# Optimization experiments

Measured on AMD Instinct MI355X. Metric: run time of the kernel, lower is better.

Reference implementation:

```python
import jax, jax.numpy as jnp
import numpy as np

N_NODES = 100_000
N_EDGES = 3_200_000
N_FEAT = 128
HIDDEN = 16
OUT = 2
N_GRAPHS = 64


def setup_inputs() -> dict:
    key = jax.random.key(0)
    ks = jax.random.split(key, 12)
    x = jax.random.normal(ks[0], (N_NODES, N_FEAT), dtype=jnp.float32)
    edge_index = jax.random.randint(ks[1], (2, N_EDGES), 0, N_NODES, dtype=jnp.int64)
    batch_idx = jnp.sort(jax.random.randint(ks[2], (N_NODES,), 0, N_GRAPHS, dtype=jnp.int64))

    def glorot(k, shape):
        s = jnp.sqrt(6.0 / (shape[0] + shape[1])).astype(jnp.float32)
        return jax.random.uniform(k, shape, jnp.float32, -1.0, 1.0) * s

    return {
        "x": x, "edge_index": edge_index, "batch_idx": batch_idx,
        "W0": glorot(ks[3], (N_FEAT, HIDDEN)), "b0": jnp.zeros((HIDDEN,), jnp.float32),
        "a0": jnp.full((1,), 0.25, jnp.float32),  # PReLU default weight
        "W1": glorot(ks[4], (HIDDEN, HIDDEN)), "b1": jnp.zeros((HIDDEN,), jnp.float32),
        "a1": jnp.full((1,), 0.25, jnp.float32),
        "W2": glorot(ks[5], (HIDDEN, HIDDEN)), "b2": jnp.zeros((HIDDEN,), jnp.float32),
        "a2": jnp.full((1,), 0.25, jnp.float32),
        "W3": glorot(ks[6], (HIDDEN, OUT)), "b3": jnp.zeros((OUT,), jnp.float32),
    }


def _prelu(x, a):
    return jnp.where(x > 0, x, a * x)


def _gcn_conv(x, W, b, src, dst, norm, n):
    # PyG GCNConv: linear transform, then normalized gather-scatter aggregation, then bias
    h = x @ W                                   # [N, out]
    msg = h[src] * norm[:, None]                # gather + per-edge scale
    out = jax.ops.segment_sum(msg, dst, num_segments=n)  # scatter-add into targets
    return out + b


def reference(x, edge_index, batch_idx, W0, b0, a0, W1, b1, a1, W2, b2, a2, W3, b3):
    n = x.shape[0]
    loop = jnp.arange(n, dtype=edge_index.dtype)
    src = jnp.concatenate([edge_index[0], loop])  # add self loops
    dst = jnp.concatenate([edge_index[1], loop])
    # symmetric degree normalization deg^-1/2 (deg over targets, all edge weights = 1)
    deg = jax.ops.segment_sum(jnp.ones_like(dst, dtype=x.dtype), dst, num_segments=n)
    dinv = jnp.where(deg > 0, jax.lax.rsqrt(deg), 0.0)
    norm = dinv[src] * dinv[dst]

    h = _prelu(_gcn_conv(x, W0, b0, src, dst, norm, n), a0)
    h = _prelu(_gcn_conv(h, W1, b1, src, dst, norm, n), a1)
    h = _prelu(_gcn_conv(h, W2, b2, src, dst, norm, n), a2)
    h = _gcn_conv(h, W3, b3, src, dst, norm, n)

    # global_mean_pool over graph ids
    sums = jax.ops.segment_sum(h, batch_idx, num_segments=N_GRAPHS)
    cnts = jax.ops.segment_sum(jnp.ones((n,), h.dtype), batch_idx, num_segments=N_GRAPHS)
    return sums / jnp.maximum(cnts, 1.0)[:, None]
```

## Files before the change

kernel.cpp:

```cpp
#include <hip/hip_runtime.h>


#define NN 100000
#define NE 3200000
#define NF 128
#define NH 16
#define NO 2
#define NG 64
#define NBLK 391
#define BN 256
#define NBUK 391
#define CHUNK 4096
#define NBLKA 782
#define CAPF 10240
#define NT0 6250

typedef __attribute__((ext_vector_type(8))) short short8;
typedef __attribute__((ext_vector_type(4))) float float4v;


__device__ __forceinline__ float ldf(const void* p, int i, int f32) {
  if (f32) return ((const float*)p)[i];
  unsigned int u = ((const unsigned short*)p)[i];
  return __uint_as_float(u << 16);
}
__device__ __forceinline__ int ldi(const void* p, int i, int i64) {
  if (i64) return (int)((const long long*)p)[i];
  return ((const int*)p)[i];
}
__device__ __forceinline__ void stf(void* p, int i, float v, int f32) {
  if (f32) {
    ((float*)p)[i] = v;
  } else {
    unsigned int w = __float_as_uint(v);
    unsigned int r = (w + 0x7fffu + ((w >> 16) & 1u)) >> 16;
    ((unsigned short*)p)[i] = (unsigned short)r;
  }
}
__device__ __forceinline__ float bf16lo(unsigned int u) { return __uint_as_float(u << 16); }
__device__ __forceinline__ float bf16hi(unsigned int u) { return __uint_as_float(u & 0xffff0000u); }
__device__ __forceinline__ unsigned int packbf(float x, float y) {
  unsigned int a = __float_as_uint(x);
  a = (a + 0x7fffu + ((a >> 16) & 1u)) >> 16;
  unsigned int b = __float_as_uint(y);
  b = (b + 0x7fffu + ((b >> 16) & 1u)) & 0xffff0000u;
  return a | b;
}
__device__ __forceinline__ int okf(float v) { return (v == v) && (fabsf(v) < 1e30f); }
__device__ __forceinline__ void nflag(int* diag, int bad, int bit) {
  if (__any(bad)) {
    if ((threadIdx.x & 63) == 0) atomicOr(diag + 2, 1 << bit);
  }
}
__device__ __forceinline__ int clampi(int v, int hi) {
  return (unsigned)v < (unsigned)hi ? v : 0;
}


__global__ __launch_bounds__(64) void k_sniff(const void* x, const void* ei, int* diag) {
  int lane = threadIdx.x;
  unsigned int xv = ((const unsigned int*)x)[lane];
  unsigned int e = (xv >> 7) & 0xffu;
  int hit = (e >= 116u && e <= 133u);
  int hits = __popcll(__ballot(hit));
  unsigned int ev = ((const unsigned int*)ei)[2 * lane + 1];
  int nzc = __popcll(__ballot(ev != 0u));
  if (lane == 0) {
    diag[0] = (hits < 32) ? 1 : 0;
    diag[1] = (nzc == 0) ? 1 : 0;
  }
}


__global__ __launch_bounds__(256) void k_build(const void* ei, const int* __restrict__ diag,
                                               int* __restrict__ cursor, int* __restrict__ ents) {
  __shared__ int spktA[CHUNK];
  __shared__ unsigned short sbid[CHUNK];
  __shared__ unsigned short srank[CHUNK];
  __shared__ int spktB[CHUNK];
  __shared__ int gpos[CHUNK];
  __shared__ int lscan[512];
  __shared__ int sexcl[NBUK];
  __shared__ int goff[NBUK];
  int tid = threadIdx.x, blk = blockIdx.x;
  lscan[tid] = 0; lscan[tid + 256] = 0;
  __syncthreads();
  int i64 = diag[1];
  int base = blk * CHUNK;
  int n = NE - base; n = n > CHUNK ? CHUNK : n;
  for (int i = tid; i < n; i += 256) {
    int sv = clampi(ldi(ei, base + i, i64), NN);
    int dv = clampi(ldi(ei, NE + base + i, i64), NN);
    int b = dv >> 8;
    spktA[i] = ((dv & 255) << 17) | sv;
    sbid[i] = (unsigned short)b;
    srank[i] = (unsigned short)atomicAdd(&lscan[b], 1);
  }
  __syncthreads();
  for (int off = 1; off < 512; off <<= 1) {
    int v0 = (tid >= off) ? lscan[tid - off] : 0;
    int v1 = lscan[tid + 256 - off];
    __syncthreads();
    lscan[tid] += v0;
    lscan[tid + 256] += v1;
    __syncthreads();
  }
  for (int b = tid; b < NBUK; b += 256) {
    int incl = lscan[b];
    int excl = (b > 0) ? lscan[b - 1] : 0;
    int cnt = incl - excl;
    sexcl[b] = excl;
    int rbase = cnt ? atomicAdd(&cursor[b], cnt) : 0;
    goff[b] = b * CAPF + rbase - excl;
  }
  __syncthreads();
  for (int i = tid; i < n; i += 256) {
    int b = sbid[i];
    int rr = sexcl[b] + srank[i];
    spktB[rr] = spktA[i];
    int gp = goff[b] + rr;
    int hi = b * CAPF + CAPF - 1;
    gpos[rr] = gp <= hi ? gp : hi;
  }
  __syncthreads();
  for (int r = tid; r < n; r += 256) ents[gpos[r]] = spktB[r];
}

__global__ __launch_bounds__(256) void k_bsort(int* __restrict__ ents, const int* __restrict__ cursor,
                                               int* __restrict__ rowstart, int* __restrict__ rowend,
                                               float* __restrict__ dinv, int* __restrict__ diag) {
  __shared__ int ent[CAPF];
  __shared__ unsigned short rnk[CAPF];
  __shared__ int lcnt[BN];
  __shared__ int sexcl[BN];
  int tid = threadIdx.x, b = blockIdx.x;
  int bs = b * CAPF;
  int n = cursor[b];
  if (n > CAPF) { n = CAPF; if (tid == 0) atomicOr(diag + 2, 1 << 9); }
  lcnt[tid] = 0;
  __syncthreads();
  for (int i = tid; i < n; i += 256) {
    int e = ents[bs + i];
    ent[i] = e;
    rnk[i] = (unsigned short)atomicAdd(&lcnt[e >> 17], 1);
  }
  __syncthreads();
  int c = lcnt[tid];
  for (int off = 1; off < 256; off <<= 1) {
    int v = (tid >= off) ? lcnt[tid - off] : 0;
    __syncthreads();
    lcnt[tid] += v;
    __syncthreads();
  }
  int excl = lcnt[tid] - c;
  sexcl[tid] = excl;
  int node = (b << 8) + tid;
  if (node < NN) {
    rowstart[node] = bs + excl;
    rowend[node] = bs + excl + c;
    dinv[node] = rsqrtf((float)(c + 1));
  }
  __syncthreads();
  for (int i = tid; i < n; i += 256) {
    int e = ent[i];
    ents[bs + sexcl[e >> 17] + rnk[i]] = e & 0x1FFFF;
  }
}


__global__ __launch_bounds__(256) void k_t0(const void* __restrict__ x, const void* __restrict__ W0,
                                            const float* __restrict__ dinv,
                                            int* __restrict__ diag, unsigned int* __restrict__ out) {
  __shared__ float ws[NF * NH];
  __shared__ float xs[16 * 129];
  int tid = threadIdx.x;
  int f32 = diag[0];
  if (!f32) {
    const unsigned short* xu = (const unsigned short*)x;
    const unsigned short* wu = (const unsigned short*)W0;
    int wave = tid >> 6, lane = tid & 63;
    int nfe = lane & 15, quad = lane >> 4;
    short8 bfr[4];
#pragma unroll
    for (int mf = 0; mf < 4; ++mf) {
      short8 t;
#pragma unroll
      for (int j = 0; j < 8; ++j) t[j] = (short)wu[(mf * 32 + quad * 8 + j) * NH + nfe];
      bfr[mf] = t;
    }
    int tile = blockIdx.x * 4 + wave;
    if (tile < NT0) {
      int node0 = tile * 16;
      const short8* xrow = (const short8*)(xu + (node0 + nfe) * NF);
      float4v c = {0.f, 0.f, 0.f, 0.f};
#pragma unroll
      for (int mf = 0; mf < 4; ++mf) {
        short8 a = xrow[mf * 4 + quad];
        c = __builtin_amdgcn_mfma_f32_16x16x32_bf16(a, bfr[mf], c, 0, 0, 0);
      }
      int bad = 0;
#pragma unroll
      for (int r = 0; r < 4; ++r) {
        int node = node0 + quad * 4 + r;
        float v = c[r] * dinv[node];
        float o = __shfl_xor(v, 1);
        if (!(nfe & 1)) out[node * 8 + (nfe >> 1)] = packbf(v, o);
        bad |= !okf(v);
      }
      nflag(diag, bad, 0);
    }
  } else {
    for (int t = 0; t < 4; ++t) {
      int tile = blockIdx.x * 4 + t;
      if (tile >= NT0) break;
      int node0 = tile * 16;
      __syncthreads();
#pragma unroll
      for (int r = 0; r < 8; ++r) ws[tid + 256 * r] = ldf(W0, tid + 256 * r, 1);
#pragma unroll
      for (int r = 0; r < 8; ++r) {
        int idx = tid + 256 * r;
        int row = idx >> 7, col = idx & 127;
        xs[row * 129 + col] = ldf(x, (node0 + row) * NF + col, 1);
      }
      __syncthreads();
      int nl = tid >> 4, f = tid & 15;
      float acc = 0.f;
#pragma unroll 4
      for (int k = 0; k < NF; ++k) acc += xs[nl * 129 + k] * ws[k * NH + f];
      acc *= dinv[node0 + nl];
      float other = __shfl_xor(acc, 1);
      if ((f & 1) == 0) out[(node0 + nl) * 8 + (f >> 1)] = packbf(acc, other);
      nflag(diag, !okf(acc), 0);
    }
  }
}


__global__ __launch_bounds__(256) void k_aggT(const uint2* __restrict__ hin,
                                              const int* __restrict__ srcs,
                                              const int* __restrict__ rowstart,
                                              const int* __restrict__ rowend,
                                              const float* __restrict__ dinv,
                                              const void* __restrict__ b, const void* __restrict__ a,
                                              const void* __restrict__ Wn,
                                              int* __restrict__ diag, int bit,
                                              uint2* __restrict__ hout) {
  __shared__ float ws[NH * NH];
  int tid = threadIdx.x;
  int f32 = diag[0];
  ws[tid] = ldf(Wn, tid, f32);
  __syncthreads();
  int gid = blockIdx.x * 256 + tid;
  if (gid >= NN * 4) return;
  int node = gid >> 2, p = gid & 3;
  uint2 self = hin[gid];
  float acc0 = bf16lo(self.x), acc1 = bf16hi(self.x);
  float acc2 = bf16lo(self.y), acc3 = bf16hi(self.y);
  int e = rowstart[node], e1 = rowend[node];
  for (; e + 4 <= e1; e += 4) {
    int s0 = srcs[e], s1 = srcs[e + 1], s2 = srcs[e + 2], s3 = srcs[e + 3];
    uint2 v0 = hin[s0 * 4 + p];
    uint2 v1 = hin[s1 * 4 + p];
    uint2 v2 = hin[s2 * 4 + p];
    uint2 v3 = hin[s3 * 4 + p];
    acc0 += bf16lo(v0.x) + bf16lo(v1.x) + bf16lo(v2.x) + bf16lo(v3.x);
    acc1 += bf16hi(v0.x) + bf16hi(v1.x) + bf16hi(v2.x) + bf16hi(v3.x);
    acc2 += bf16lo(v0.y) + bf16lo(v1.y) + bf16lo(v2.y) + bf16lo(v3.y);
    acc3 += bf16hi(v0.y) + bf16hi(v1.y) + bf16hi(v2.y) + bf16hi(v3.y);
  }
  for (; e < e1; ++e) {
    uint2 v = hin[srcs[e] * 4 + p];
    acc0 += bf16lo(v.x);
    acc1 += bf16hi(v.x);
    acc2 += bf16lo(v.y);
    acc3 += bf16hi(v.y);
  }
  float dv = dinv[node];
  float av = ldf(a, 0, f32);
  float p0 = dv * acc0 + ldf(b, 4 * p + 0, f32);
  float p1 = dv * acc1 + ldf(b, 4 * p + 1, f32);
  float p2 = dv * acc2 + ldf(b, 4 * p + 2, f32);
  float p3 = dv * acc3 + ldf(b, 4 * p + 3, f32);
  p0 = p0 > 0.f ? p0 : av * p0;
  p1 = p1 > 0.f ? p1 : av * p1;
  p2 = p2 > 0.f ? p2 : av * p2;
  p3 = p3 > 0.f ? p3 : av * p3;
  float t0 = 0.f, t1 = 0.f, t2 = 0.f, t3 = 0.f;
#pragma unroll
  for (int j = 0; j < 4; ++j) {
    float q0 = __shfl(p0, j, 4);
    float q1 = __shfl(p1, j, 4);
    float q2 = __shfl(p2, j, 4);
    float q3 = __shfl(p3, j, 4);
    const float* w0 = &ws[(4 * j) * NH + 4 * p];
    const float* w1 = &ws[(4 * j + 1) * NH + 4 * p];
    const float* w2 = &ws[(4 * j + 2) * NH + 4 * p];
    const float* w3 = &ws[(4 * j + 3) * NH + 4 * p];
    t0 += q0 * w0[0] + q1 * w1[0] + q2 * w2[0] + q3 * w3[0];
    t1 += q0 * w0[1] + q1 * w1[1] + q2 * w2[1] + q3 * w3[1];
    t2 += q0 * w0[2] + q1 * w1[2] + q2 * w2[2] + q3 * w3[2];
    t3 += q0 * w0[3] + q1 * w1[3] + q2 * w2[3] + q3 * w3[3];
  }
  t0 *= dv; t1 *= dv; t2 *= dv; t3 *= dv;
  uint2 o;
  o.x = packbf(t0, t1);
  o.y = packbf(t2, t3);
  hout[gid] = o;
  nflag(diag, !okf(t0) || !okf(t3), bit);
}

__global__ __launch_bounds__(256) void k_aggT3(const uint2* __restrict__ hin,
                                               const int* __restrict__ srcs,
                                               const int* __restrict__ rowstart,
                                               const int* __restrict__ rowend,
                                               const float* __restrict__ dinv,
                                               const void* __restrict__ b, const void* __restrict__ a,
                                               const void* __restrict__ W3,
                                               int* __restrict__ diag, float2* __restrict__ hout) {
  __shared__ float ws[NH * NO];
  int tid = threadIdx.x;
  int f32 = diag[0];
  if (tid < NH * NO) ws[tid] = ldf(W3, tid, f32);
  __syncthreads();
  int gid = blockIdx.x * 256 + tid;
  if (gid >= NN * 4) return;
  int node = gid >> 2, p = gid & 3;
  uint2 self = hin[gid];
  float acc0 = bf16lo(self.x), acc1 = bf16hi(self.x);
  float acc2 = bf16lo(self.y), acc3 = bf16hi(self.y);
  int e = rowstart[node], e1 = rowend[node];
  for (; e + 4 <= e1; e += 4) {
    int s0 = srcs[e], s1 = srcs[e + 1], s2 = srcs[e + 2], s3 = srcs[e + 3];
    uint2 v0 = hin[s0 * 4 + p];
    uint2 v1 = hin[s1 * 4 + p];
    uint2 v2 = hin[s2 * 4 + p];
    uint2 v3 = hin[s3 * 4 + p];
    acc0 += bf16lo(v0.x) + bf16lo(v1.x) + bf16lo(v2.x) + bf16lo(v3.x);
    acc1 += bf16hi(v0.x) + bf16hi(v1.x) + bf16hi(v2.x) + bf16hi(v3.x);
    acc2 += bf16lo(v0.y) + bf16lo(v1.y) + bf16lo(v2.y) + bf16lo(v3.y);
    acc3 += bf16hi(v0.y) + bf16hi(v1.y) + bf16hi(v2.y) + bf16hi(v3.y);
  }
  for (; e < e1; ++e) {
    uint2 v = hin[srcs[e] * 4 + p];
    acc0 += bf16lo(v.x);
    acc1 += bf16hi(v.x);
    acc2 += bf16lo(v.y);
    acc3 += bf16hi(v.y);
  }
  float dv = dinv[node];
  float av = ldf(a, 0, f32);
  float p0 = dv * acc0 + ldf(b, 4 * p + 0, f32);
  float p1 = dv * acc1 + ldf(b, 4 * p + 1, f32);
  float p2 = dv * acc2 + ldf(b, 4 * p + 2, f32);
  float p3 = dv * acc3 + ldf(b, 4 * p + 3, f32);
  p0 = p0 > 0.f ? p0 : av * p0;
  p1 = p1 > 0.f ? p1 : av * p1;
  p2 = p2 > 0.f ? p2 : av * p2;
  p3 = p3 > 0.f ? p3 : av * p3;
  float u0 = p0 * ws[(4 * p) * NO]     + p1 * ws[(4 * p + 1) * NO] +
             p2 * ws[(4 * p + 2) * NO] + p3 * ws[(4 * p + 3) * NO];
  float u1 = p0 * ws[(4 * p) * NO + 1]     + p1 * ws[(4 * p + 1) * NO + 1] +
             p2 * ws[(4 * p + 2) * NO + 1] + p3 * ws[(4 * p + 3) * NO + 1];
  u0 += __shfl_xor(u0, 1, 4);
  u0 += __shfl_xor(u0, 2, 4);
  u1 += __shfl_xor(u1, 1, 4);
  u1 += __shfl_xor(u1, 2, 4);
  if (p == 0) hout[node] = make_float2(dv * u0, dv * u1);
  nflag(diag, !okf(u0) || !okf(u1), 6);
}

__global__ __launch_bounds__(256) void k_agg2p(const float2* __restrict__ tin,
                                               const int* __restrict__ srcs,
                                               const int* __restrict__ rowstart,
                                               const int* __restrict__ rowend,
                                               const float* __restrict__ dinv,
                                               const void* __restrict__ b3,
                                               const void* __restrict__ batch,
                                               int* __restrict__ diag, float* __restrict__ pool) {
  __shared__ float ssum[NG * NO];
  __shared__ float scnt[NG];
  int tid = threadIdx.x;
  int f32 = diag[0], i64 = diag[1];
  if (tid < NG * NO) ssum[tid] = 0.f;
  if (tid < NG) scnt[tid] = 0.f;
  __syncthreads();
  int node = blockIdx.x * 256 + tid;
  if (node < NN) {
    float2 t = tin[node];
    float a0 = t.x, a1 = t.y;
    int e = rowstart[node], e1 = rowend[node];
    for (; e + 4 <= e1; e += 4) {
      int s0 = srcs[e], s1 = srcs[e + 1], s2 = srcs[e + 2], s3 = srcs[e + 3];
      float2 h0 = tin[s0], h1 = tin[s1], h2 = tin[s2], h3 = tin[s3];
      a0 += h0.x + h1.x + h2.x + h3.x;
      a1 += h0.y + h1.y + h2.y + h3.y;
    }
    for (; e < e1; ++e) {
      float2 hv = tin[srcs[e]];
      a0 += hv.x;
      a1 += hv.y;
    }
    float dv = dinv[node];
    a0 = dv * a0 + ldf(b3, 0, f32);
    a1 = dv * a1 + ldf(b3, 1, f32);
    int g = ldi(batch, node, i64);
    g = (unsigned)g < NG ? g : 0;
    atomicAdd(&ssum[g * 2], a0);
    atomicAdd(&ssum[g * 2 + 1], a1);
    atomicAdd(&scnt[g], 1.f);
    nflag(diag, !okf(a0) || !okf(a1), 7);
  }
  __syncthreads();
  if (tid < NG * NO && ssum[tid] != 0.f) atomicAdd(&pool[tid], ssum[tid]);
  if (tid < NG && scnt[tid] != 0.f) atomicAdd(&pool[NG * NO + tid], scnt[tid]);
}

__global__ __launch_bounds__(128) void k_final(const float* __restrict__ pool,
                                               const int* __restrict__ diag, void* __restrict__ out) {
  int i = threadIdx.x;
  int f32 = diag[0], i64 = diag[1], stg = diag[2];
  float c = pool[NG * NO + (i >> 1)];
  c = c > 1.f ? c : 1.f;
  float v = pool[i] / c;
  if (stg != 0 || !okf(v)) {
    int stage = stg ? __ffs(stg) : 15;
    v = 1024.0f + stage * 64.0f + f32 * 16.0f + i64 * 8.0f;
  }
  stf(out, i, v, f32);
}

__global__ __launch_bounds__(128) void k_diag_ws(void* out, float v) {
  unsigned int w = __float_as_uint(v);
  ((unsigned short*)out)[threadIdx.x] = (unsigned short)(w >> 16);
}


extern "C" void kernel_launch(void* const* d_in, const int* in_sizes, int n_in,
                              void* d_out, int out_size, void* d_ws, size_t ws_size,
                              hipStream_t stream) {
  const void* x  = d_in[0];
  const void* ei = d_in[1];
  const void* batch = d_in[2];
  const void* W0 = d_in[3];
  const void* b0 = d_in[4];
  const void* a0 = d_in[5];
  const void* W1 = d_in[6];
  const void* b1 = d_in[7];
  const void* a1 = d_in[8];
  const void* W2 = d_in[9];
  const void* b2 = d_in[10];
  const void* a2 = d_in[11];
  const void* W3 = d_in[12];
  const void* b3 = d_in[13];

  char* w = (char*)d_ws;
  int* diag         = (int*)(w + 0);
  float* pool       = (float*)(w + 64);
  int* cursor       = (int*)(w + 896);
  float* dinv       = (float*)(w + 2496);
  int* rowstart     = (int*)(w + 402496);
  int* rowend       = (int*)(w + 802496);
  int* ents         = (int*)(w + 1202496);
  uint2* hsA        = (uint2*)(w + 17217856);
  uint2* hsB        = (uint2*)(w + 20417856);
  float2* hs3       = (float2*)(w + 23617856);
  const size_t NEED = 24417856;

  if (ws_size < NEED) {
    k_diag_ws<<<1, 128, 0, stream>>>(d_out, (float)ws_size);
    return;
  }

  hipMemsetAsync(d_ws, 0, 2496, stream);

  k_sniff<<<1, 64, 0, stream>>>(x, ei, diag);

  k_build<<<NBLKA, 256, 0, stream>>>(ei, diag, cursor, ents);
  k_bsort<<<NBUK, 256, 0, stream>>>(ents, cursor, rowstart, rowend, dinv, diag);

  k_t0<<<(NT0 + 3) / 4, 256, 0, stream>>>(x, W0, dinv, diag, (unsigned int*)hsA);
  k_aggT<<<(NN * 4 + 255) / 256, 256, 0, stream>>>(hsA, ents, rowstart, rowend, dinv, b0, a0, W1, diag, 1, hsB);
  k_aggT<<<(NN * 4 + 255) / 256, 256, 0, stream>>>(hsB, ents, rowstart, rowend, dinv, b1, a1, W2, diag, 3, hsA);
  k_aggT3<<<(NN * 4 + 255) / 256, 256, 0, stream>>>(hsA, ents, rowstart, rowend, dinv, b2, a2, W3, diag, hs3);
  k_agg2p<<<NBLK, 256, 0, stream>>>(hs3, ents, rowstart, rowend, dinv, b3, batch, diag, pool);

  k_final<<<1, 128, 0, stream>>>(pool, diag, d_out);
}
```

Baseline: 323.6 us.

## Fold workspace memset into sniff kernel, widen build blocks, deepen gather unroll

The separate hipMemsetAsync of the diagnostics, pool and cursor region is removed, and the k_sniff kernel now zeroes those 624 ints itself before writing its flags, which saves one stream operation. k_build and k_bsort go from 256 to 512 threads per block, so the 512-entry scan becomes one element per thread and the bucket loops take a wider stride. The neighbour gather loops in the aggregation kernels unroll by 8 instead of 4, issuing more independent loads before accumulating, with 2-wide and single-element tails. The risks are higher register pressure in the aggregation kernels and lower occupancy for the 512-thread blocks that use a lot of shared memory.

```diff
diff --git a/kernel.cpp b/kernel.cpp
--- a/kernel.cpp
+++ b/kernel.cpp
@@ -57,22 +57,26 @@
 }
 
 
-__global__ __launch_bounds__(64) void k_sniff(const void* x, const void* ei, int* diag) {
-  int lane = threadIdx.x;
-  unsigned int xv = ((const unsigned int*)x)[lane];
-  unsigned int e = (xv >> 7) & 0xffu;
-  int hit = (e >= 116u && e <= 133u);
-  int hits = __popcll(__ballot(hit));
-  unsigned int ev = ((const unsigned int*)ei)[2 * lane + 1];
-  int nzc = __popcll(__ballot(ev != 0u));
-  if (lane == 0) {
-    diag[0] = (hits < 32) ? 1 : 0;
-    diag[1] = (nzc == 0) ? 1 : 0;
-  }
-}
-
-
-__global__ __launch_bounds__(256) void k_build(const void* ei, const int* __restrict__ diag,
+__global__ __launch_bounds__(1024) void k_sniff(const void* x, const void* ei, int* zbase) {
+  int tid = threadIdx.x;
+  if (tid < 624) zbase[tid] = 0;
+  __syncthreads();
+  if (tid < 64) {
+    unsigned int xv = ((const unsigned int*)x)[tid];
+    unsigned int e = (xv >> 7) & 0xffu;
+    int hit = (e >= 116u && e <= 133u);
+    int hits = __popcll(__ballot(hit));
+    unsigned int ev = ((const unsigned int*)ei)[2 * tid + 1];
+    int nzc = __popcll(__ballot(ev != 0u));
+    if (tid == 0) {
+      zbase[0] = (hits < 32) ? 1 : 0;
+      zbase[1] = (nzc == 0) ? 1 : 0;
+    }
+  }
+}
+
+
+__global__ __launch_bounds__(512) void k_build(const void* ei, const int* __restrict__ diag,
                                                int* __restrict__ cursor, int* __restrict__ ents) {
   __shared__ int spktA[CHUNK];
   __shared__ unsigned short sbid[CHUNK];
@@ -83,12 +87,12 @@
   __shared__ int sexcl[NBUK];
   __shared__ int goff[NBUK];
   int tid = threadIdx.x, blk = blockIdx.x;
-  lscan[tid] = 0; lscan[tid + 256] = 0;
+  lscan[tid] = 0;
   __syncthreads();
   int i64 = diag[1];
   int base = blk * CHUNK;
   int n = NE - base; n = n > CHUNK ? CHUNK : n;
-  for (int i = tid; i < n; i += 256) {
+  for (int i = tid; i < n; i += 512) {
     int sv = clampi(ldi(ei, base + i, i64), NN);
     int dv = clampi(ldi(ei, NE + base + i, i64), NN);
     int b = dv >> 8;
@@ -98,14 +102,13 @@
   }
   __syncthreads();
   for (int off = 1; off < 512; off <<= 1) {
-    int v0 = (tid >= off) ? lscan[tid - off] : 0;
-    int v1 = lscan[tid + 256 - off];
+    int v = (tid >= off) ? lscan[tid - off] : 0;
     __syncthreads();
-    lscan[tid] += v0;
-    lscan[tid + 256] += v1;
+    lscan[tid] += v;
     __syncthreads();
   }
-  for (int b = tid; b < NBUK; b += 256) {
+  if (tid < NBUK) {
+    int b = tid;
     int incl = lscan[b];
     int excl = (b > 0) ? lscan[b - 1] : 0;
     int cnt = incl - excl;
@@ -114,7 +117,7 @@
     goff[b] = b * CAPF + rbase - excl;
   }
   __syncthreads();
-  for (int i = tid; i < n; i += 256) {
+  for (int i = tid; i < n; i += 512) {
     int b = sbid[i];
     int rr = sexcl[b] + srank[i];
     spktB[rr] = spktA[i];
@@ -123,10 +126,10 @@
     gpos[rr] = gp <= hi ? gp : hi;
   }
   __syncthreads();
-  for (int r = tid; r < n; r += 256) ents[gpos[r]] = spktB[r];
-}
-
-__global__ __launch_bounds__(256) void k_bsort(int* __restrict__ ents, const int* __restrict__ cursor,
+  for (int r = tid; r < n; r += 512) ents[gpos[r]] = spktB[r];
+}
+
+__global__ __launch_bounds__(512) void k_bsort(int* __restrict__ ents, const int* __restrict__ cursor,
                                                int* __restrict__ rowstart, int* __restrict__ rowend,
                                                float* __restrict__ dinv, int* __restrict__ diag) {
   __shared__ int ent[CAPF];
@@ -137,31 +140,33 @@
   int bs = b * CAPF;
   int n = cursor[b];
   if (n > CAPF) { n = CAPF; if (tid == 0) atomicOr(diag + 2, 1 << 9); }
-  lcnt[tid] = 0;
-  __syncthreads();
-  for (int i = tid; i < n; i += 256) {
+  if (tid < BN) lcnt[tid] = 0;
+  __syncthreads();
+  for (int i = tid; i < n; i += 512) {
     int e = ents[bs + i];
     ent[i] = e;
     rnk[i] = (unsigned short)atomicAdd(&lcnt[e >> 17], 1);
   }
   __syncthreads();
-  int c = lcnt[tid];
-  for (int off = 1; off < 256; off <<= 1) {
-    int v = (tid >= off) ? lcnt[tid - off] : 0;
+  int c = (tid < BN) ? lcnt[tid] : 0;
+  for (int off = 1; off < BN; off <<= 1) {
+    int v = (tid < BN && tid >= off) ? lcnt[tid - off] : 0;
     __syncthreads();
-    lcnt[tid] += v;
+    if (tid < BN) lcnt[tid] += v;
     __syncthreads();
   }
-  int excl = lcnt[tid] - c;
-  sexcl[tid] = excl;
-  int node = (b << 8) + tid;
-  if (node < NN) {
-    rowstart[node] = bs + excl;
-    rowend[node] = bs + excl + c;
-    dinv[node] = rsqrtf((float)(c + 1));
-  }
-  __syncthreads();
-  for (int i = tid; i < n; i += 256) {
+  if (tid < BN) {
+    int excl = lcnt[tid] - c;
+    sexcl[tid] = excl;
+    int node = (b << 8) + tid;
+    if (node < NN) {
+      rowstart[node] = bs + excl;
+      rowend[node] = bs + excl + c;
+      dinv[node] = rsqrtf((float)(c + 1));
+    }
+  }
+  __syncthreads();
+  for (int i = tid; i < n; i += 512) {
     int e = ent[i];
     ents[bs + sexcl[e >> 17] + rnk[i]] = e & 0x1FFFF;
   }
@@ -258,18 +263,27 @@
   float acc0 = bf16lo(self.x), acc1 = bf16hi(self.x);
   float acc2 = bf16lo(self.y), acc3 = bf16hi(self.y);
   int e = rowstart[node], e1 = rowend[node];
-  for (; e + 4 <= e1; e += 4) {
-    int s0 = srcs[e], s1 = srcs[e + 1], s2 = srcs[e + 2], s3 = srcs[e + 3];
-    uint2 v0 = hin[s0 * 4 + p];
-    uint2 v1 = hin[s1 * 4 + p];
-    uint2 v2 = hin[s2 * 4 + p];
-    uint2 v3 = hin[s3 * 4 + p];
-    acc0 += bf16lo(v0.x) + bf16lo(v1.x) + bf16lo(v2.x) + bf16lo(v3.x);
-    acc1 += bf16hi(v0.x) + bf16hi(v1.x) + bf16hi(v2.x) + bf16hi(v3.x);
-    acc2 += bf16lo(v0.y) + bf16lo(v1.y) + bf16lo(v2.y) + bf16lo(v3.y);
-    acc3 += bf16hi(v0.y) + bf16hi(v1.y) + bf16hi(v2.y) + bf16hi(v3.y);
-  }
-  for (; e < e1; ++e) {
+  for (; e + 8 <= e1; e += 8) {
+    uint2 v[8];
+#pragma unroll
+    for (int k = 0; k < 8; ++k) v[k] = hin[srcs[e + k] * 4 + p];
+#pragma unroll
+    for (int k = 0; k < 8; ++k) {
+      acc0 += bf16lo(v[k].x);
+      acc1 += bf16hi(v[k].x);
+      acc2 += bf16lo(v[k].y);
+      acc3 += bf16hi(v[k].y);
+    }
+  }
+  for (; e + 2 <= e1; e += 2) {
+    uint2 va = hin[srcs[e] * 4 + p];
+    uint2 vb = hin[srcs[e + 1] * 4 + p];
+    acc0 += bf16lo(va.x) + bf16lo(vb.x);
+    acc1 += bf16hi(va.x) + bf16hi(vb.x);
+    acc2 += bf16lo(va.y) + bf16lo(vb.y);
+    acc3 += bf16hi(va.y) + bf16hi(vb.y);
+  }
+  if (e < e1) {
     uint2 v = hin[srcs[e] * 4 + p];
     acc0 += bf16lo(v.x);
     acc1 += bf16hi(v.x);
@@ -330,18 +344,27 @@
   float acc0 = bf16lo(self.x), acc1 = bf16hi(self.x);
   float acc2 = bf16lo(self.y), acc3 = bf16hi(self.y);
   int e = rowstart[node], e1 = rowend[node];
-  for (; e + 4 <= e1; e += 4) {
-    int s0 = srcs[e], s1 = srcs[e + 1], s2 = srcs[e + 2], s3 = srcs[e + 3];
-    uint2 v0 = hin[s0 * 4 + p];
-    uint2 v1 = hin[s1 * 4 + p];
-    uint2 v2 = hin[s2 * 4 + p];
-    uint2 v3 = hin[s3 * 4 + p];
-    acc0 += bf16lo(v0.x) + bf16lo(v1.x) + bf16lo(v2.x) + bf16lo(v3.x);
-    acc1 += bf16hi(v0.x) + bf16hi(v1.x) + bf16hi(v2.x) + bf16hi(v3.x);
-    acc2 += bf16lo(v0.y) + bf16lo(v1.y) + bf16lo(v2.y) + bf16lo(v3.y);
-    acc3 += bf16hi(v0.y) + bf16hi(v1.y) + bf16hi(v2.y) + bf16hi(v3.y);
-  }
-  for (; e < e1; ++e) {
+  for (; e + 8 <= e1; e += 8) {
+    uint2 v[8];
+#pragma unroll
+    for (int k = 0; k < 8; ++k) v[k] = hin[srcs[e + k] * 4 + p];
+#pragma unroll
+    for (int k = 0; k < 8; ++k) {
+      acc0 += bf16lo(v[k].x);
+      acc1 += bf16hi(v[k].x);
+      acc2 += bf16lo(v[k].y);
+      acc3 += bf16hi(v[k].y);
+    }
+  }
+  for (; e + 2 <= e1; e += 2) {
+    uint2 va = hin[srcs[e] * 4 + p];
+    uint2 vb = hin[srcs[e + 1] * 4 + p];
+    acc0 += bf16lo(va.x) + bf16lo(vb.x);
+    acc1 += bf16hi(va.x) + bf16hi(vb.x);
+    acc2 += bf16lo(va.y) + bf16lo(vb.y);
+    acc3 += bf16hi(va.y) + bf16hi(vb.y);
+  }
+  if (e < e1) {
     uint2 v = hin[srcs[e] * 4 + p];
     acc0 += bf16lo(v.x);
     acc1 += bf16hi(v.x);
@@ -472,12 +495,10 @@
     return;
   }
 
-  hipMemsetAsync(d_ws, 0, 2496, stream);
-
-  k_sniff<<<1, 64, 0, stream>>>(x, ei, diag);
-
-  k_build<<<NBLKA, 256, 0, stream>>>(ei, diag, cursor, ents);
-  k_bsort<<<NBUK, 256, 0, stream>>>(ents, cursor, rowstart, rowend, dinv, diag);
+  k_sniff<<<1, 1024, 0, stream>>>(x, ei, (int*)w);
+
+  k_build<<<NBLKA, 512, 0, stream>>>(ei, diag, cursor, ents);
+  k_bsort<<<NBUK, 512, 0, stream>>>(ents, cursor, rowstart, rowend, dinv, diag);
 
   k_t0<<<(NT0 + 3) / 4, 256, 0, stream>>>(x, W0, dinv, diag, (unsigned int*)hsA);
   k_aggT<<<(NN * 4 + 255) / 256, 256, 0, stream>>>(hsA, ents, rowstart, rowend, dinv, b0, a0, W1, diag, 1, hsB);
```

New measurement: 302.2 us. 1.07x faster.
